# Performance work log

Hardware: AMD Instinct MI355X
Metric: run time of the kernel (lower is better)

Reference implementation:

```python
import jax, jax.numpy as jnp
import numpy as np
import math

NUM_HEADS = 16
ROPE_BASE = 10000.0
SLIDING_WINDOW = 512  # note: original triu-then-tril composition makes the mask empty (no-op)


def _rope_cos_sin(seq_len, head_dim, dtype):
    inv_freq = 1.0 / (ROPE_BASE ** (jnp.arange(0, head_dim, 2, dtype=jnp.float32) / head_dim))
    t = jnp.arange(seq_len, dtype=jnp.float32)
    freqs = t[:, None] * inv_freq[None, :]          # [S, D/2]
    emb = jnp.concatenate([freqs, freqs], axis=-1)  # [S, D]
    # reshape to broadcast over [B, S, H, D]
    return jnp.cos(emb)[None, :, None, :].astype(dtype), jnp.sin(emb)[None, :, None, :].astype(dtype)


def _rotate_half(x):
    x1, x2 = jnp.split(x, 2, axis=-1)
    return jnp.concatenate([-x2, x1], axis=-1)


def setup_inputs() -> dict:
    key = jax.random.key(0)
    ks = jax.random.split(key, 9)
    B, S, E = 2, 2048, 2048
    sc = 1.0 / math.sqrt(E)
    return {
        "hidden_states": jax.random.normal(ks[0], (B, S, E), dtype=jnp.float32),
        "Wq": jax.random.normal(ks[1], (E, E), dtype=jnp.float32) * sc,
        "bq": jax.random.normal(ks[2], (E,), dtype=jnp.float32) * 0.01,
        "Wk": jax.random.normal(ks[3], (E, E), dtype=jnp.float32) * sc,
        "bk": jax.random.normal(ks[4], (E,), dtype=jnp.float32) * 0.01,
        "Wv": jax.random.normal(ks[5], (E, E), dtype=jnp.float32) * sc,
        "bv": jax.random.normal(ks[6], (E,), dtype=jnp.float32) * 0.01,
        "Wo": jax.random.normal(ks[7], (E, E), dtype=jnp.float32) * sc,
        "bo": jax.random.normal(ks[8], (E,), dtype=jnp.float32) * 0.01,
    }


def reference(hidden_states, Wq, bq, Wk, bk, Wv, bv, Wo, bo):
    B, S, E = hidden_states.shape
    H = NUM_HEADS
    D = E // H
    q = (hidden_states @ Wq.T + bq).reshape(B, S, H, D)
    k = (hidden_states @ Wk.T + bk).reshape(B, S, H, D)
    v = (hidden_states @ Wv.T + bv).reshape(B, S, H, D)

    cos, sin = _rope_cos_sin(S, D, q.dtype)
    q = q * cos + _rotate_half(q) * sin
    k = k * cos + _rotate_half(k) * sin

    scale = 1.0 / math.sqrt(D)
    scores = jnp.einsum("bqhd,bkhd->bhqk", q, k) * scale  # [B,H,S,S]
    # Faithful to source: triu(ones, +w) followed by tril(..., -w) is empty -> mask is a no-op.
    attn = jax.nn.softmax(scores, axis=-1)
    out = jnp.einsum("bhqk,bkhd->bqhd", attn, v).reshape(B, S, E)
    return out @ Wo.T + bo
```

## Files before the change

kernel.cpp:

```cpp
#include <hip/hip_runtime.h>
#include <hip/hip_bf16.h>

#define B_ 2
#define S_ 2048
#define E_ 2048
#define H_ 16
#define D_ 128
#define M_ (B_*S_)
#define NQKV_ (3*E_)

typedef __attribute__((ext_vector_type(8))) short bf16x8;
typedef __attribute__((ext_vector_type(4))) float f32x4;
typedef __attribute__((ext_vector_type(4))) unsigned short u16x4;
typedef __attribute__((ext_vector_type(2))) unsigned u32x2;

__device__ __forceinline__ unsigned short f2bf(float f) {
  union { float f; unsigned u; } v; v.f = f;
  unsigned r = v.u + 0x7fffu + ((v.u >> 16) & 1u);
  return (unsigned short)(r >> 16);
}
__device__ __forceinline__ float bf2f(unsigned short h) {
  union { unsigned u; float f; } v; v.u = ((unsigned)h) << 16;
  return v.f;
}

__device__ __forceinline__ void gload_lds16(const void* g, void* l) {
  __builtin_amdgcn_global_load_lds(
      (const __attribute__((address_space(1))) unsigned*)g,
      (__attribute__((address_space(3))) unsigned*)l, 16, 0, 0);
}

__global__ __launch_bounds__(256) void prep_kernel(
    const float* __restrict__ hs,
    const float* __restrict__ Wq, const float* __restrict__ Wk, const float* __restrict__ Wv,
    const float* __restrict__ Wo,
    const float* __restrict__ bq, const float* __restrict__ bk, const float* __restrict__ bv,
    unsigned short* __restrict__ hsb, unsigned short* __restrict__ Wqkv,
    unsigned short* __restrict__ Wob, float* __restrict__ biasqkv,
    float* __restrict__ cosT, float* __restrict__ sinT)
{
  const int seg = blockIdx.y;
  const int t0 = blockIdx.x * 256 + threadIdx.x;
  const int stride = gridDim.x * 256;
  if (seg == 0) {
    const int n = (M_*E_)/4;
    for (int i = t0; i < n; i += stride) {
      f32x4 v = ((const f32x4*)hs)[i];
      u16x4 o; o[0]=f2bf(v[0]); o[1]=f2bf(v[1]); o[2]=f2bf(v[2]); o[3]=f2bf(v[3]);
      ((u16x4*)hsb)[i] = o;
    }
  } else if (seg == 1) {
    const int n = (3*E_*E_)/4;
    for (int i = t0; i < n; i += stride) {
      int e4 = i << 2;
      int r = e4 >> 11;
      int k = e4 & 2047;
      const float* src = (r < E_) ? (Wq + ((size_t)r << 11) + k)
                       : (r < 2*E_) ? (Wk + ((size_t)(r - E_) << 11) + k)
                       : (Wv + ((size_t)(r - 2*E_) << 11) + k);
      f32x4 v = *(const f32x4*)src;
      u16x4 o; o[0]=f2bf(v[0]); o[1]=f2bf(v[1]); o[2]=f2bf(v[2]); o[3]=f2bf(v[3]);
      ((u16x4*)Wqkv)[i] = o;
    }
  } else if (seg == 2) {
    const int n = (E_*E_)/4;
    for (int i = t0; i < n; i += stride) {
      f32x4 v = ((const f32x4*)Wo)[i];
      u16x4 o; o[0]=f2bf(v[0]); o[1]=f2bf(v[1]); o[2]=f2bf(v[2]); o[3]=f2bf(v[3]);
      ((u16x4*)Wob)[i] = o;
    }
  } else if (seg == 3) {
    for (int i = t0; i < NQKV_; i += stride)
      biasqkv[i] = (i < E_) ? bq[i] : (i < 2*E_) ? bk[i - E_] : bv[i - 2*E_];
  } else {
    for (int i = t0; i < S_*64; i += stride) {
      int j = i & 63, s = i >> 6;
      float inv = exp2f(-(float)j * (13.287712379549449f / 64.0f));
      float ang = (float)s * inv;
      cosT[i] = cosf(ang);
      sinT[i] = sinf(ang);
    }
  }
}

#define STAGE8(basePtr, BUF, AB, KS, KT) do { \
    unsigned short* dst_ = lds + (BUF)*32768 + (AB)*16384 + (KS)*8192; \
    const unsigned short* src_ = (basePtr) + (KT)*64 + (KS)*32; \
    _Pragma("unroll") \
    for (int j_ = 0; j_ < 2; ++j_) { \
      int cc_ = (j_ << 9) + tid; \
      int row_ = cc_ >> 2, c2_ = cc_ & 3; \
      int sc_ = c2_ ^ ((row_ >> 1) & 3); \
      gload_lds16(src_ + (size_t)row_*K + sc_*8, (char*)dst_ + cc_*16); \
    } } while(0)

#define LOADA8(MH, KS, BUF) do { \
    const unsigned short* Ab_ = lds + (BUF)*32768 + (KS)*8192; \
    _Pragma("unroll") \
    for (int j_ = 0; j_ < 4; ++j_) { \
      int row_ = wr*128 + ((MH)*4 + j_)*16 + l15; \
      af[j_] = *(const bf16x8*)(Ab_ + row_*32 + ((l4 ^ ((row_>>1)&3)) << 3)); \
    } } while(0)

#define LOADB8(KS, BUF) do { \
    const unsigned short* Bb_ = lds + (BUF)*32768 + 16384 + (KS)*8192; \
    _Pragma("unroll") \
    for (int j_ = 0; j_ < 4; ++j_) { \
      int row_ = wc*64 + j_*16 + l15; \
      bf[j_] = *(const bf16x8*)(Bb_ + row_*32 + ((l4 ^ ((row_>>1)&3)) << 3)); \
    } } while(0)

#define MFMAQ(MH) do { \
    _Pragma("unroll") \
    for (int mm_ = 0; mm_ < 4; ++mm_) \
      _Pragma("unroll") \
      for (int nn_ = 0; nn_ < 4; ++nn_) \
        acc[(MH)*4+mm_][nn_] = __builtin_amdgcn_mfma_f32_16x16x32_bf16(af[mm_], bf[nn_], acc[(MH)*4+mm_][nn_], 0,0,0); \
  } while(0)

#define WVM6 asm volatile("s_waitcnt vmcnt(6)" ::: "memory")
#define WVM0 asm volatile("s_waitcnt vmcnt(0)" ::: "memory")

#define PHASE(MH, KS, BUF, ISSUE, WAITV) do { \
    LOADA8(MH, KS, BUF); \
    if ((MH) == 0) LOADB8(KS, BUF); \
    ISSUE; \
    __builtin_amdgcn_sched_barrier(0); \
    __builtin_amdgcn_s_barrier(); \
    asm volatile("s_waitcnt lgkmcnt(0)" ::: "memory"); \
    __builtin_amdgcn_sched_barrier(0); \
    __builtin_amdgcn_s_setprio(1); \
    MFMAQ(MH); \
    __builtin_amdgcn_s_setprio(0); \
    WAITV; \
    __builtin_amdgcn_s_barrier(); \
  } while(0)

__global__ __launch_bounds__(512, 2) void gemm8(
    const unsigned short* __restrict__ A,
    const unsigned short* __restrict__ Bm,
    const float* __restrict__ bias,
    unsigned short* __restrict__ Cv,
    int M, int N, int K)
{
  __shared__ __align__(16) unsigned short lds[65536];
  const int tid = threadIdx.x;
  const int lane = tid & 63;
  const int w = tid >> 6;
  const int wr = w >> 2, wc = w & 3;
  const int l15 = lane & 15, l4 = lane >> 4;

  const int ntile = N >> 8;
  int wg = blockIdx.x;
  const int cpx = gridDim.x >> 3;
  wg = (wg & 7) * cpx + (wg >> 3);
  const int tm = wg / ntile, tn = wg % ntile;

  const unsigned short* Abase = A + ((size_t)tm*256)*K;
  const unsigned short* Bbase = Bm + ((size_t)tn*256)*K;

  f32x4 acc[8][4] = {};
  bf16x8 af[4], bf[4];

  const int NITER = K >> 7;

  STAGE8(Bbase, 0, 1, 0, 0); STAGE8(Abase, 0, 0, 0, 0);
  STAGE8(Bbase, 0, 1, 1, 0); STAGE8(Abase, 0, 0, 1, 0);
  STAGE8(Bbase, 1, 1, 0, 1); STAGE8(Abase, 1, 0, 0, 1);
  STAGE8(Bbase, 1, 1, 1, 1);
  __builtin_amdgcn_sched_barrier(0);
  WVM6;
  __builtin_amdgcn_s_barrier();

  for (int i = 0; i < NITER; ++i) {
    const int t1k = 2*i + 1, t2k = 2*i + 2, t3k = 2*i + 3;
    const bool nl = (i < NITER - 1);
    PHASE(0, 0, 0, STAGE8(Abase, 1, 0, 1, t1k), );
    PHASE(1, 0, 0, if (nl) STAGE8(Bbase, 0, 1, 0, t2k), );
    PHASE(0, 1, 0, if (nl) STAGE8(Abase, 0, 0, 0, t2k), );
    PHASE(1, 1, 0, if (nl) STAGE8(Bbase, 0, 1, 1, t2k), if (nl) WVM6; else WVM0);
    PHASE(0, 0, 1, if (nl) STAGE8(Abase, 0, 0, 1, t2k), );
    PHASE(1, 0, 1, if (nl) STAGE8(Bbase, 1, 1, 0, t3k), );
    PHASE(0, 1, 1, if (nl) STAGE8(Abase, 1, 0, 0, t3k), );
    PHASE(1, 1, 1, if (nl) STAGE8(Bbase, 1, 1, 1, t3k), if (nl) WVM6);
  }

  #pragma unroll
  for (int mt = 0; mt < 8; ++mt) {
    #pragma unroll
    for (int nt = 0; nt < 4; ++nt) {
      int colg = tn*256 + wc*64 + nt*16 + l15;
      float bvv = bias[colg];
      #pragma unroll
      for (int r = 0; r < 4; ++r) {
        int rowg = tm*256 + wr*128 + mt*16 + l4*4 + r;
        Cv[(size_t)rowg*N + colg] = f2bf(acc[mt][nt][r] + bvv);
      }
    }
  }
}

template<int OUT_F32>
__global__ __launch_bounds__(256) void gemm_bt(
    const unsigned short* __restrict__ A,
    const unsigned short* __restrict__ Bm,
    const float* __restrict__ bias,
    void* __restrict__ Cv,
    int M, int N, int K)
{
  __shared__ unsigned short lA[128*64];
  __shared__ unsigned short lB[128*64];
  const int tid = threadIdx.x;
  const int lane = tid & 63;
  const int w = tid >> 6;
  const int wr = w >> 1, wc = w & 1;
  const int ntile = N >> 7;
  const int tm = blockIdx.x / ntile, tn = blockIdx.x % ntile;
  const int l15 = lane & 15, l4 = lane >> 4;

  f32x4 acc[4][4] = {};

  for (int kt = 0; kt < K; kt += 64) {
    #pragma unroll
    for (int i = 0; i < 4; ++i) {
      int cc = i*256 + tid;
      int row = cc >> 3, col = cc & 7;
      int scol = col ^ (row & 7);
      gload_lds16(A + (size_t)(tm*128 + row)*K + kt + scol*8, (char*)lA + cc*16);
    }
    #pragma unroll
    for (int i = 0; i < 4; ++i) {
      int cc = i*256 + tid;
      int row = cc >> 3, col = cc & 7;
      int scol = col ^ (row & 7);
      gload_lds16(Bm + (size_t)(tn*128 + row)*K + kt + scol*8, (char*)lB + cc*16);
    }
    asm volatile("s_waitcnt vmcnt(0)" ::: "memory");
    __syncthreads();

    #pragma unroll
    for (int ks = 0; ks < 2; ++ks) {
      bf16x8 af[4], bfr[4];
      #pragma unroll
      for (int mt = 0; mt < 4; ++mt) {
        int row = wr*64 + mt*16 + l15;
        int ch = (ks*4 + l4) ^ (row & 7);
        af[mt] = *(const bf16x8*)(lA + row*64 + ch*8);
      }
      #pragma unroll
      for (int nt = 0; nt < 4; ++nt) {
        int row = wc*64 + nt*16 + l15;
        int ch = (ks*4 + l4) ^ (row & 7);
        bfr[nt] = *(const bf16x8*)(lB + row*64 + ch*8);
      }
      #pragma unroll
      for (int mt = 0; mt < 4; ++mt)
        #pragma unroll
        for (int nt = 0; nt < 4; ++nt)
          acc[mt][nt] = __builtin_amdgcn_mfma_f32_16x16x32_bf16(af[mt], bfr[nt], acc[mt][nt], 0, 0, 0);
    }
    __syncthreads();
  }

  #pragma unroll
  for (int mt = 0; mt < 4; ++mt) {
    #pragma unroll
    for (int nt = 0; nt < 4; ++nt) {
      int colg = tn*128 + wc*64 + nt*16 + l15;
      float bvv = bias[colg];
      #pragma unroll
      for (int r = 0; r < 4; ++r) {
        int rowg = tm*128 + wr*64 + mt*16 + l4*4 + r;
        float v = acc[mt][nt][r] + bvv;
        if (OUT_F32) ((float*)Cv)[(size_t)rowg*N + colg] = v;
        else ((unsigned short*)Cv)[(size_t)rowg*N + colg] = f2bf(v);
      }
    }
  }
}

__global__ __launch_bounds__(256) void rope_kernel(
    unsigned short* __restrict__ qkv, const float* __restrict__ cosT, const float* __restrict__ sinT)
{
  int t = blockIdx.x*256 + threadIdx.x;
  int i  = t & 63;
  int h  = (t >> 6) & 15;
  int m  = t >> 10;
  int s  = m & (S_-1);
  float c = cosT[s*64 + i], sn = sinT[s*64 + i];
  const float scale = 0.08838834764831845f * 1.4426950408889634f;
  size_t base = (size_t)m*NQKV_ + h*128;
  float q1 = bf2f(qkv[base+i]), q2 = bf2f(qkv[base+64+i]);
  qkv[base+i]    = f2bf((q1*c - q2*sn)*scale);
  qkv[base+64+i] = f2bf((q2*c + q1*sn)*scale);
  size_t kb = base + E_;
  float k1 = bf2f(qkv[kb+i]), k2 = bf2f(qkv[kb+64+i]);
  qkv[kb+i]    = f2bf(k1*c - k2*sn);
  qkv[kb+64+i] = f2bf(k2*c + k1*sn);
}

__global__ __launch_bounds__(256) void transv_kernel(
    const unsigned short* __restrict__ qkv, unsigned short* __restrict__ Vt)
{
  __shared__ unsigned short t[32][33];
  int bid = blockIdx.x;
  int st = bid & 63;
  int dt = (bid >> 6) & 3;
  int bh = bid >> 8;
  int b = bh >> 4, h = bh & 15;
  int tx = threadIdx.x & 31, ty = threadIdx.x >> 5;
  #pragma unroll
  for (int j = 0; j < 4; ++j) {
    int r = ty + j*8;
    t[r][tx] = qkv[(size_t)(b*S_ + st*32 + r)*NQKV_ + 2*E_ + h*128 + dt*32 + tx];
  }
  __syncthreads();
  #pragma unroll
  for (int j = 0; j < 4; ++j) {
    int r = ty + j*8;
    Vt[((size_t)bh*D_ + dt*32 + r)*S_ + st*32 + tx] = t[tx][r];
  }
}

__global__ __launch_bounds__(256, 2) void attn_kernel(
    const unsigned short* __restrict__ qkv, const unsigned short* __restrict__ Vt,
    unsigned short* __restrict__ Ao)
{
  __shared__ unsigned short lK[64*128];
  __shared__ unsigned short lV[128*64];
  __shared__ __align__(16) unsigned short lP[4*32*64];
  int bid = blockIdx.x;
  bid = (bid & 7)*64 + (bid >> 3);
  const int qt = bid & 15;
  const int bh = bid >> 4;
  const int b = bh >> 4, h = bh & 15;
  const int tid = threadIdx.x, lane = tid & 63, w = tid >> 6;
  const int l15 = lane & 15, l4 = lane >> 4;

  bf16x8 qf[2][4];
  #pragma unroll
  for (int g = 0; g < 2; ++g) {
    const int qrow = qt*128 + w*32 + g*16 + l15;
    const unsigned short* qp = qkv + (size_t)(b*S_ + qrow)*NQKV_ + h*128 + l4*8;
    #pragma unroll
    for (int f = 0; f < 4; ++f) qf[g][f] = *(const bf16x8*)(qp + f*32);
  }

  f32x4 O[2][8];
  #pragma unroll
  for (int g = 0; g < 2; ++g)
    #pragma unroll
    for (int i = 0; i < 8; ++i) O[g][i] = (f32x4){0.f,0.f,0.f,0.f};
  float mx[2] = {-1e30f,-1e30f}, lsum[2] = {0.f,0.f};

  unsigned short* myP = lP + w*(32*64);
  const int ksw = (l15 & 7) << 3;
  const size_t kbase = (size_t)b*S_*NQKV_ + E_ + (size_t)h*128;
  const size_t vbase = (size_t)bh*D_*S_;

  for (int kt = 0; kt < S_; kt += 64) {
    #pragma unroll
    for (int i = 0; i < 4; ++i) {
      int cc = i*256 + tid;
      int row = cc >> 4, col = cc & 15;
      int scol = col ^ (row & 7);
      gload_lds16(qkv + kbase + (size_t)(kt + row)*NQKV_ + scol*8, (char*)lK + cc*16);
    }
    #pragma unroll
    for (int i = 0; i < 4; ++i) {
      int cc = i*256 + tid;
      int row = cc >> 3, col = cc & 7;
      int scol = col ^ ((row & 7) ^ ((row >> 3) & 7));
      gload_lds16(Vt + vbase + (size_t)row*S_ + kt + scol*8, (char*)lV + cc*16);
    }
    asm volatile("s_waitcnt vmcnt(0)" ::: "memory");
    __syncthreads();

    f32x4 sfr[2][4];
    #pragma unroll
    for (int nf = 0; nf < 4; ++nf) {
      f32x4 s0 = (f32x4){0.f,0.f,0.f,0.f};
      f32x4 s1 = (f32x4){0.f,0.f,0.f,0.f};
      #pragma unroll
      for (int ks = 0; ks < 4; ++ks) {
        int row = nf*16 + l15;
        int ch = (ks*4 + l4) ^ (row & 7);
        bf16x8 kf = *(const bf16x8*)(lK + row*128 + ch*8);
        s0 = __builtin_amdgcn_mfma_f32_16x16x32_bf16(kf, qf[0][ks], s0, 0, 0, 0);
        s1 = __builtin_amdgcn_mfma_f32_16x16x32_bf16(kf, qf[1][ks], s1, 0, 0, 0);
      }
      sfr[0][nf] = s0; sfr[1][nf] = s1;
    }

    float vm[2];
    #pragma unroll
    for (int g = 0; g < 2; ++g) {
      float v = -1e30f;
      #pragma unroll
      for (int nf = 0; nf < 4; ++nf)
        #pragma unroll
        for (int r = 0; r < 4; ++r) v = fmaxf(v, sfr[g][nf][r]);
      v = fmaxf(v, __shfl_xor(v, 16, 64));
      v = fmaxf(v, __shfl_xor(v, 32, 64));
      vm[g] = v;
    }

    if (__any((vm[0] > mx[0] + 8.0f) || (vm[1] > mx[1] + 8.0f))) {
      #pragma unroll
      for (int g = 0; g < 2; ++g) {
        float mn = fmaxf(mx[g], vm[g]);
        float al = __builtin_amdgcn_exp2f(mx[g] - mn);
        mx[g] = mn;
        lsum[g] *= al;
        #pragma unroll
        for (int r = 0; r < 4; ++r) {
          float ar = __shfl(al, (lane & 48) + l4*4 + r, 64);
          #pragma unroll
          for (int df = 0; df < 8; ++df) O[g][df][r] *= ar;
        }
      }
    }

    #pragma unroll
    for (int g = 0; g < 2; ++g) {
      float ps = 0.f;
      #pragma unroll
      for (int nf = 0; nf < 4; ++nf) {
        #pragma unroll
        for (int r = 0; r < 4; ++r) {
          float p = __builtin_amdgcn_exp2f(sfr[g][nf][r] - mx[g]);
          sfr[g][nf][r] = p;
          ps += p;
        }
      }
      ps += __shfl_xor(ps, 16, 64);
      ps += __shfl_xor(ps, 32, 64);
      lsum[g] += ps;
    }

    #pragma unroll
    for (int g = 0; g < 2; ++g) {
      #pragma unroll
      for (int nf = 0; nf < 4; ++nf) {
        unsigned lo = (unsigned)f2bf(sfr[g][nf][0]) | ((unsigned)f2bf(sfr[g][nf][1]) << 16);
        unsigned hi = (unsigned)f2bf(sfr[g][nf][2]) | ((unsigned)f2bf(sfr[g][nf][3]) << 16);
        int k0 = (nf*16 + l4*4) ^ ksw;
        u32x2 val; val[0] = lo; val[1] = hi;
        *(u32x2*)(myP + (g*16 + l15)*64 + k0) = val;
      }
    }
    asm volatile("s_waitcnt lgkmcnt(0)" ::: "memory");

    #pragma unroll
    for (int ks2 = 0; ks2 < 2; ++ks2) {
      int kk = (ks2*32 + l4*8) ^ ksw;
      bf16x8 pf0 = *(const bf16x8*)(myP + l15*64 + kk);
      bf16x8 pf1 = *(const bf16x8*)(myP + (16 + l15)*64 + kk);
      #pragma unroll
      for (int df = 0; df < 8; ++df) {
        int row = df*16 + l15;
        int ch = (ks2*4 + l4) ^ ((row & 7) ^ ((row >> 3) & 7));
        bf16x8 vf = *(const bf16x8*)(lV + row*64 + ch*8);
        O[0][df] = __builtin_amdgcn_mfma_f32_16x16x32_bf16(pf0, vf, O[0][df], 0, 0, 0);
        O[1][df] = __builtin_amdgcn_mfma_f32_16x16x32_bf16(pf1, vf, O[1][df], 0, 0, 0);
      }
    }
    __syncthreads();
  }

  #pragma unroll
  for (int g = 0; g < 2; ++g) {
    float linv = 1.0f / lsum[g];
    float inv[4];
    #pragma unroll
    for (int r = 0; r < 4; ++r) inv[r] = __shfl(linv, (lane & 48) + l4*4 + r, 64);
    #pragma unroll
    for (int df = 0; df < 8; ++df) {
      int colg = h*128 + df*16 + l15;
      #pragma unroll
      for (int r = 0; r < 4; ++r) {
        int rowg = qt*128 + w*32 + g*16 + l4*4 + r;
        Ao[(size_t)(b*S_ + rowg)*E_ + colg] = f2bf(O[g][df][r] * inv[r]);
      }
    }
  }
}

extern "C" void kernel_launch(void* const* d_in, const int* in_sizes, int n_in,
                              void* d_out, int out_size, void* d_ws, size_t ws_size,
                              hipStream_t stream) {
  const float* hs = (const float*)d_in[0];
  const float* Wq = (const float*)d_in[1];
  const float* bq = (const float*)d_in[2];
  const float* Wk = (const float*)d_in[3];
  const float* bk = (const float*)d_in[4];
  const float* Wv = (const float*)d_in[5];
  const float* bv = (const float*)d_in[6];
  const float* Wo = (const float*)d_in[7];
  const float* bo = (const float*)d_in[8];
  float* out = (float*)d_out;

  char* p = (char*)d_ws;
  auto alloc = [&](size_t bytes) { char* r = p; p += (bytes + 255) & ~(size_t)255; return r; };
  unsigned short* hsb  = (unsigned short*)alloc((size_t)M_*E_*2);
  unsigned short* Wqkv = (unsigned short*)alloc((size_t)NQKV_*E_*2);
  unsigned short* Wob  = (unsigned short*)alloc((size_t)E_*E_*2);
  unsigned short* qkv  = (unsigned short*)alloc((size_t)M_*NQKV_*2);
  unsigned short* Vt   = (unsigned short*)alloc((size_t)B_*H_*D_*S_*2);
  unsigned short* Ao   = (unsigned short*)alloc((size_t)M_*E_*2);
  float* biasqkv = (float*)alloc((size_t)NQKV_*4);
  float* cosT = (float*)alloc((size_t)S_*64*4);
  float* sinT = (float*)alloc((size_t)S_*64*4);

  prep_kernel<<<dim3(2048, 5), 256, 0, stream>>>(hs, Wq, Wk, Wv, Wo, bq, bk, bv,
      hsb, Wqkv, Wob, biasqkv, cosT, sinT);
  gemm8<<<dim3((M_/256)*(NQKV_/256)), 512, 0, stream>>>(hsb, Wqkv, biasqkv, qkv, M_, NQKV_, E_);
  rope_kernel<<<dim3((M_*H_*64)/256), 256, 0, stream>>>(qkv, cosT, sinT);
  transv_kernel<<<dim3(B_*H_*(D_/32)*(S_/32)), 256, 0, stream>>>(qkv, Vt);
  attn_kernel<<<dim3(B_*H_*(S_/128)), 256, 0, stream>>>(qkv, Vt, Ao);
  gemm_bt<1><<<dim3((M_/128)*(E_/128)), 256, 0, stream>>>(Ao, Wob, bo, out, M_, E_, E_);
}
```

Measured before the change: 297.6 us.

## Replace both GEMMs with unified 128x256 triple-buffered pipelined kernel

Drops the 256x256 QKV GEMM and the simple 128x128 output-projection GEMM and replaces both with one templated 128x256-tile, 512-thread kernel. The new kernel uses three LDS buffers with loads issued two k-tiles ahead. The QKV GEMM now gets more workgroups (smaller M tile), which improves wave balance across CUs. The output projection now gets the pipelined, swizzled, XCD-remapped kernel in place of the synchronous one. The cost is a smaller tile for QKV, which lowers per-tile data reuse, plus a larger LDS footprint per block.

```diff
diff --git a/kernel.cpp b/kernel.cpp
--- a/kernel.cpp
+++ b/kernel.cpp
@@ -83,190 +83,104 @@
   }
 }
 
-#define STAGE8(basePtr, BUF, AB, KS, KT) do { \
-    unsigned short* dst_ = lds + (BUF)*32768 + (AB)*16384 + (KS)*8192; \
-    const unsigned short* src_ = (basePtr) + (KT)*64 + (KS)*32; \
+#define STGA(BUFP, TKT, KS) do { \
+    unsigned short* dst_ = lds + (BUFP)*24576 + (KS)*4096; \
+    const unsigned short* src_ = Abase + (TKT)*64 + (KS)*32; \
+    int cc_ = tid; int row_ = cc_ >> 2, c2_ = cc_ & 3; \
+    int sc_ = c2_ ^ ((row_ >> 1) & 3); \
+    gload_lds16(src_ + (size_t)row_*K + sc_*8, (char*)dst_ + cc_*16); \
+  } while(0)
+
+#define STGB(BUFP, TKT, KS) do { \
+    unsigned short* dst_ = lds + (BUFP)*24576 + 8192 + (KS)*8192; \
+    const unsigned short* src_ = Bbase + (TKT)*64 + (KS)*32; \
     _Pragma("unroll") \
     for (int j_ = 0; j_ < 2; ++j_) { \
-      int cc_ = (j_ << 9) + tid; \
-      int row_ = cc_ >> 2, c2_ = cc_ & 3; \
+      int cc_ = (j_ << 9) + tid; int row_ = cc_ >> 2, c2_ = cc_ & 3; \
       int sc_ = c2_ ^ ((row_ >> 1) & 3); \
       gload_lds16(src_ + (size_t)row_*K + sc_*8, (char*)dst_ + cc_*16); \
     } } while(0)
 
-#define LOADA8(MH, KS, BUF) do { \
-    const unsigned short* Ab_ = lds + (BUF)*32768 + (KS)*8192; \
-    _Pragma("unroll") \
-    for (int j_ = 0; j_ < 4; ++j_) { \
-      int row_ = wr*128 + ((MH)*4 + j_)*16 + l15; \
-      af[j_] = *(const bf16x8*)(Ab_ + row_*32 + ((l4 ^ ((row_>>1)&3)) << 3)); \
-    } } while(0)
-
-#define LOADB8(KS, BUF) do { \
-    const unsigned short* Bb_ = lds + (BUF)*32768 + 16384 + (KS)*8192; \
-    _Pragma("unroll") \
-    for (int j_ = 0; j_ < 4; ++j_) { \
-      int row_ = wc*64 + j_*16 + l15; \
-      bf[j_] = *(const bf16x8*)(Bb_ + row_*32 + ((l4 ^ ((row_>>1)&3)) << 3)); \
-    } } while(0)
-
-#define MFMAQ(MH) do { \
-    _Pragma("unroll") \
-    for (int mm_ = 0; mm_ < 4; ++mm_) \
+#define PHA(KS, BUF, ISSUE, WAITV) do { \
+    { const unsigned short* Ab_ = lds + (BUF)*24576 + (KS)*4096; \
       _Pragma("unroll") \
-      for (int nn_ = 0; nn_ < 4; ++nn_) \
-        acc[(MH)*4+mm_][nn_] = __builtin_amdgcn_mfma_f32_16x16x32_bf16(af[mm_], bf[nn_], acc[(MH)*4+mm_][nn_], 0,0,0); \
-  } while(0)
-
-#define WVM6 asm volatile("s_waitcnt vmcnt(6)" ::: "memory")
-#define WVM0 asm volatile("s_waitcnt vmcnt(0)" ::: "memory")
-
-#define PHASE(MH, KS, BUF, ISSUE, WAITV) do { \
-    LOADA8(MH, KS, BUF); \
-    if ((MH) == 0) LOADB8(KS, BUF); \
+      for (int j_ = 0; j_ < 4; ++j_) { \
+        int row_ = wr*64 + j_*16 + l15; \
+        af[j_] = *(const bf16x8*)(Ab_ + row_*32 + ((l4 ^ ((row_>>1)&3)) << 3)); } \
+      const unsigned short* Bb_ = lds + (BUF)*24576 + 8192 + (KS)*8192; \
+      _Pragma("unroll") \
+      for (int j_ = 0; j_ < 4; ++j_) { \
+        int row_ = wc*64 + j_*16 + l15; \
+        bf[j_] = *(const bf16x8*)(Bb_ + row_*32 + ((l4 ^ ((row_>>1)&3)) << 3)); } } \
     ISSUE; \
     __builtin_amdgcn_sched_barrier(0); \
     __builtin_amdgcn_s_barrier(); \
     asm volatile("s_waitcnt lgkmcnt(0)" ::: "memory"); \
     __builtin_amdgcn_sched_barrier(0); \
     __builtin_amdgcn_s_setprio(1); \
-    MFMAQ(MH); \
+    _Pragma("unroll") \
+    for (int mm_ = 0; mm_ < 4; ++mm_) \
+      _Pragma("unroll") \
+      for (int nn_ = 0; nn_ < 4; ++nn_) \
+        acc[mm_][nn_] = __builtin_amdgcn_mfma_f32_16x16x32_bf16(af[mm_], bf[nn_], acc[mm_][nn_], 0,0,0); \
     __builtin_amdgcn_s_setprio(0); \
     WAITV; \
     __builtin_amdgcn_s_barrier(); \
   } while(0)
 
-__global__ __launch_bounds__(512, 2) void gemm8(
-    const unsigned short* __restrict__ A,
-    const unsigned short* __restrict__ Bm,
-    const float* __restrict__ bias,
-    unsigned short* __restrict__ Cv,
-    int M, int N, int K)
-{
-  __shared__ __align__(16) unsigned short lds[65536];
-  const int tid = threadIdx.x;
-  const int lane = tid & 63;
-  const int w = tid >> 6;
-  const int wr = w >> 2, wc = w & 3;
-  const int l15 = lane & 15, l4 = lane >> 4;
-
-  const int ntile = N >> 8;
-  int wg = blockIdx.x;
-  const int cpx = gridDim.x >> 3;
-  wg = (wg & 7) * cpx + (wg >> 3);
-  const int tm = wg / ntile, tn = wg % ntile;
-
-  const unsigned short* Abase = A + ((size_t)tm*256)*K;
-  const unsigned short* Bbase = Bm + ((size_t)tn*256)*K;
-
-  f32x4 acc[8][4] = {};
-  bf16x8 af[4], bf[4];
-
-  const int NITER = K >> 7;
-
-  STAGE8(Bbase, 0, 1, 0, 0); STAGE8(Abase, 0, 0, 0, 0);
-  STAGE8(Bbase, 0, 1, 1, 0); STAGE8(Abase, 0, 0, 1, 0);
-  STAGE8(Bbase, 1, 1, 0, 1); STAGE8(Abase, 1, 0, 0, 1);
-  STAGE8(Bbase, 1, 1, 1, 1);
-  __builtin_amdgcn_sched_barrier(0);
-  WVM6;
-  __builtin_amdgcn_s_barrier();
-
-  for (int i = 0; i < NITER; ++i) {
-    const int t1k = 2*i + 1, t2k = 2*i + 2, t3k = 2*i + 3;
-    const bool nl = (i < NITER - 1);
-    PHASE(0, 0, 0, STAGE8(Abase, 1, 0, 1, t1k), );
-    PHASE(1, 0, 0, if (nl) STAGE8(Bbase, 0, 1, 0, t2k), );
-    PHASE(0, 1, 0, if (nl) STAGE8(Abase, 0, 0, 0, t2k), );
-    PHASE(1, 1, 0, if (nl) STAGE8(Bbase, 0, 1, 1, t2k), if (nl) WVM6; else WVM0);
-    PHASE(0, 0, 1, if (nl) STAGE8(Abase, 0, 0, 1, t2k), );
-    PHASE(1, 0, 1, if (nl) STAGE8(Bbase, 1, 1, 0, t3k), );
-    PHASE(0, 1, 1, if (nl) STAGE8(Abase, 1, 0, 0, t3k), );
-    PHASE(1, 1, 1, if (nl) STAGE8(Bbase, 1, 1, 1, t3k), if (nl) WVM6);
-  }
-
-  #pragma unroll
-  for (int mt = 0; mt < 8; ++mt) {
-    #pragma unroll
-    for (int nt = 0; nt < 4; ++nt) {
-      int colg = tn*256 + wc*64 + nt*16 + l15;
-      float bvv = bias[colg];
-      #pragma unroll
-      for (int r = 0; r < 4; ++r) {
-        int rowg = tm*256 + wr*128 + mt*16 + l4*4 + r;
-        Cv[(size_t)rowg*N + colg] = f2bf(acc[mt][nt][r] + bvv);
-      }
-    }
-  }
-}
-
 template<int OUT_F32>
-__global__ __launch_bounds__(256) void gemm_bt(
+__global__ __launch_bounds__(512, 2) void gemmA(
     const unsigned short* __restrict__ A,
     const unsigned short* __restrict__ Bm,
     const float* __restrict__ bias,
     void* __restrict__ Cv,
     int M, int N, int K)
 {
-  __shared__ unsigned short lA[128*64];
-  __shared__ unsigned short lB[128*64];
+  __shared__ __align__(16) unsigned short lds[73728];
   const int tid = threadIdx.x;
   const int lane = tid & 63;
   const int w = tid >> 6;
-  const int wr = w >> 1, wc = w & 1;
-  const int ntile = N >> 7;
-  const int tm = blockIdx.x / ntile, tn = blockIdx.x % ntile;
+  const int wr = w >> 2, wc = w & 3;
   const int l15 = lane & 15, l4 = lane >> 4;
 
+  const int ntile = N >> 8;
+  int wg = blockIdx.x;
+  const int cpx = gridDim.x >> 3;
+  wg = (wg & 7) * cpx + (wg >> 3);
+  const int tm = wg / ntile, tn = wg % ntile;
+
+  const unsigned short* Abase = A + ((size_t)tm*128)*K;
+  const unsigned short* Bbase = Bm + ((size_t)tn*256)*K;
+
   f32x4 acc[4][4] = {};
-
-  for (int kt = 0; kt < K; kt += 64) {
-    #pragma unroll
-    for (int i = 0; i < 4; ++i) {
-      int cc = i*256 + tid;
-      int row = cc >> 3, col = cc & 7;
-      int scol = col ^ (row & 7);
-      gload_lds16(A + (size_t)(tm*128 + row)*K + kt + scol*8, (char*)lA + cc*16);
-    }
-    #pragma unroll
-    for (int i = 0; i < 4; ++i) {
-      int cc = i*256 + tid;
-      int row = cc >> 3, col = cc & 7;
-      int scol = col ^ (row & 7);
-      gload_lds16(Bm + (size_t)(tn*128 + row)*K + kt + scol*8, (char*)lB + cc*16);
-    }
-    asm volatile("s_waitcnt vmcnt(0)" ::: "memory");
-    __syncthreads();
-
-    #pragma unroll
-    for (int ks = 0; ks < 2; ++ks) {
-      bf16x8 af[4], bfr[4];
-      #pragma unroll
-      for (int mt = 0; mt < 4; ++mt) {
-        int row = wr*64 + mt*16 + l15;
-        int ch = (ks*4 + l4) ^ (row & 7);
-        af[mt] = *(const bf16x8*)(lA + row*64 + ch*8);
-      }
-      #pragma unroll
-      for (int nt = 0; nt < 4; ++nt) {
-        int row = wc*64 + nt*16 + l15;
-        int ch = (ks*4 + l4) ^ (row & 7);
-        bfr[nt] = *(const bf16x8*)(lB + row*64 + ch*8);
-      }
-      #pragma unroll
-      for (int mt = 0; mt < 4; ++mt)
-        #pragma unroll
-        for (int nt = 0; nt < 4; ++nt)
-          acc[mt][nt] = __builtin_amdgcn_mfma_f32_16x16x32_bf16(af[mt], bfr[nt], acc[mt][nt], 0, 0, 0);
-    }
-    __syncthreads();
+  bf16x8 af[4], bf[4];
+
+  const int NT = K >> 6;
+
+  STGA(0,0,0); STGB(0,0,0); STGA(0,0,1); STGB(0,0,1);
+  STGA(1,1,0); STGB(1,1,0); STGA(1,1,1); STGB(1,1,1);
+  __builtin_amdgcn_sched_barrier(0);
+  asm volatile("s_waitcnt vmcnt(6)" ::: "memory");
+  __builtin_amdgcn_s_barrier();
+  __builtin_amdgcn_sched_barrier(0);
+
+  int bufc = 0, bufn = 2;
+  for (int i = 0; i < NT; ++i) {
+    const bool st = (i + 2 < NT);
+    const bool more = (i + 1 < NT);
+    PHA(0, bufc, if (st) { STGA(bufn, i+2, 0); STGB(bufn, i+2, 0); }, );
+    PHA(1, bufc, if (st) { STGA(bufn, i+2, 1); STGB(bufn, i+2, 1); },
+        if (st) { asm volatile("s_waitcnt vmcnt(6)" ::: "memory"); }
+        else if (more) { asm volatile("s_waitcnt vmcnt(0)" ::: "memory"); });
+    bufc = (bufc + 1 == 3) ? 0 : bufc + 1;
+    bufn = (bufn + 1 == 3) ? 0 : bufn + 1;
   }
 
   #pragma unroll
   for (int mt = 0; mt < 4; ++mt) {
     #pragma unroll
     for (int nt = 0; nt < 4; ++nt) {
-      int colg = tn*128 + wc*64 + nt*16 + l15;
+      int colg = tn*256 + wc*64 + nt*16 + l15;
       float bvv = bias[colg];
       #pragma unroll
       for (int r = 0; r < 4; ++r) {
@@ -514,9 +428,9 @@
 
   prep_kernel<<<dim3(2048, 5), 256, 0, stream>>>(hs, Wq, Wk, Wv, Wo, bq, bk, bv,
       hsb, Wqkv, Wob, biasqkv, cosT, sinT);
-  gemm8<<<dim3((M_/256)*(NQKV_/256)), 512, 0, stream>>>(hsb, Wqkv, biasqkv, qkv, M_, NQKV_, E_);
+  gemmA<0><<<dim3((M_/128)*(NQKV_/256)), 512, 0, stream>>>(hsb, Wqkv, biasqkv, qkv, M_, NQKV_, E_);
   rope_kernel<<<dim3((M_*H_*64)/256), 256, 0, stream>>>(qkv, cosT, sinT);
   transv_kernel<<<dim3(B_*H_*(D_/32)*(S_/32)), 256, 0, stream>>>(qkv, Vt);
   attn_kernel<<<dim3(B_*H_*(S_/128)), 256, 0, stream>>>(qkv, Vt, Ao);
-  gemm_bt<1><<<dim3((M_/128)*(E_/128)), 256, 0, stream>>>(Ao, Wob, bo, out, M_, E_, E_);
-}
+  gemmA<1><<<dim3((M_/128)*(E_/256)), 512, 0, stream>>>(Ao, Wob, bo, out, M_, E_, E_);
+}
```

Measured after the change: 298.7 us. Within noise of the previous version (+0.4%).
